# Optimization experiments

Hardware: AMD Instinct MI355X
Metric: run time of the kernel (lower is better)

Reference implementation:

```python
import jax, jax.numpy as jnp
import numpy as np

HEADS = 8
D = 1024


def setup_inputs() -> dict:
    key = jax.random.key(0)
    ks = jax.random.split(key, 10)
    B, Sq, Sk = 8, 2048, 2048
    x = jax.random.normal(ks[0], (B, Sq, D), dtype=jnp.float32)
    context = jax.random.normal(ks[1], (B, Sk, D), dtype=jnp.float32)
    # Dense params (glorot-ish scale)
    def dense(k, fin, fout):
        return jax.random.normal(k, (fin, fout), dtype=jnp.float32) / np.sqrt(fin)
    Wq = dense(ks[2], D, HEADS); bq = jnp.zeros((HEADS,), jnp.float32)
    Wk = dense(ks[3], D, HEADS); bk = jnp.zeros((HEADS,), jnp.float32)
    Wv = dense(ks[4], D, HEADS); bv = jnp.zeros((HEADS,), jnp.float32)
    Wo = dense(ks[5], HEADS, D); bo = jnp.zeros((D,), jnp.float32)
    return {"x": x, "context": context, "Wq": Wq, "bq": bq,
            "Wk": Wk, "bk": bk, "Wv": Wv, "bv": bv, "Wo": Wo, "bo": bo}


def reference(x, context, Wq, bq, Wk, bk, Wv, bv, Wo, bo):
    # q: [B,Sq,H], k/v: [B,Sk,H]  (H = heads = projection width, no head split)
    q = jnp.einsum('bsd,dh->bsh', x, Wq) + bq
    k = jnp.einsum('btd,dh->bth', context, Wk) + bk
    v = jnp.einsum('btd,dh->bth', context, Wv) + bv
    # Dot(axes=-1): scores[b,s,t] = q[b,s,:] . k[b,t,:]  -> [B,Sq,Sk]
    scores = jnp.einsum('bsh,bth->bst', q, k)
    weights = jax.nn.softmax(scores, axis=-1)  # no 1/sqrt(d) scaling in original
    # Dot(axes=(-1,1)): out[b,s,h] = sum_t weights[b,s,t] * v[b,t,h]
    out = jnp.einsum('bst,bth->bsh', weights, v)
    return jnp.einsum('bsh,hd->bsd', out, Wo) + bo
```

## Files before the change

### kernel.cpp

```cpp
#include <hip/hip_runtime.h>

constexpr int D = 1024;
constexpr int H = 8;
constexpr int S = 2048;
constexpr int B = 8;
constexpr int NROW = B * S;

__device__ __forceinline__ int swz(int i) { return i ^ ((i >> 3) & 7); }

__global__ __launch_bounds__(512)
void proj_kernel(const float* __restrict__ x, const float* __restrict__ ctx,
                 const float* __restrict__ Wq, const float* __restrict__ bq,
                 const float* __restrict__ Wk, const float* __restrict__ bk,
                 const float* __restrict__ Wv, const float* __restrict__ bv,
                 float* __restrict__ qo, float* __restrict__ ko,
                 float* __restrict__ vo)
{
    __shared__ float4 wlds[4096];
    const int tid = threadIdx.x;
    const bool kvb = (int)blockIdx.x >= (NROW / 64);
    const int blk  = kvb ? ((int)blockIdx.x - NROW / 64) : (int)blockIdx.x;

    if (!kvb) {
        const float4* w4 = (const float4*)Wq;
        for (int i = tid; i < 2048; i += 512) wlds[swz(i)] = w4[i];
    } else {
        const float4* a4 = (const float4*)Wk;
        const float4* b4 = (const float4*)Wv;
        for (int i = tid; i < 2048; i += 512) {
            wlds[swz(i)]        = a4[i];
            wlds[2048 + swz(i)] = b4[i];
        }
    }
    __syncthreads();

    const int c    = tid & 15;
    const int team = tid >> 4;
    const int row0 = blk * 64 + team * 2;
    const float* src = kvb ? ctx : x;
    const float4* r0 = (const float4*)(src + (size_t)row0 * D);
    const float4* r1 = (const float4*)(src + (size_t)(row0 + 1) * D);

    if (!kvb) {
        float a0[8], a1[8];
#pragma unroll
        for (int h = 0; h < 8; ++h) { a0[h] = 0.f; a1[h] = 0.f; }
#pragma unroll 4
        for (int j = 0; j < 16; ++j) {
            const float4 xa = r0[16 * j + c];
            const float4 xb = r1[16 * j + c];
            const int ib = 128 * j + 8 * c;
#pragma unroll
            for (int e = 0; e < 4; ++e) {
                const float4 w0 = wlds[swz(ib + 2 * e)];
                const float4 w1 = wlds[swz(ib + 2 * e + 1)];
                const float s0 = (&xa.x)[e], s1 = (&xb.x)[e];
                a0[0] += s0 * w0.x; a0[1] += s0 * w0.y; a0[2] += s0 * w0.z; a0[3] += s0 * w0.w;
                a0[4] += s0 * w1.x; a0[5] += s0 * w1.y; a0[6] += s0 * w1.z; a0[7] += s0 * w1.w;
                a1[0] += s1 * w0.x; a1[1] += s1 * w0.y; a1[2] += s1 * w0.z; a1[3] += s1 * w0.w;
                a1[4] += s1 * w1.x; a1[5] += s1 * w1.y; a1[6] += s1 * w1.z; a1[7] += s1 * w1.w;
            }
        }
#pragma unroll
        for (int h = 0; h < 8; ++h) {
            float s0 = a0[h], s1 = a1[h];
            s0 += __shfl_down(s0, 8); s1 += __shfl_down(s1, 8);
            s0 += __shfl_down(s0, 4); s1 += __shfl_down(s1, 4);
            s0 += __shfl_down(s0, 2); s1 += __shfl_down(s1, 2);
            s0 += __shfl_down(s0, 1); s1 += __shfl_down(s1, 1);
            if (c == 0) {
                qo[(size_t)row0 * H + h]       = s0 + bq[h];
                qo[(size_t)(row0 + 1) * H + h] = s1 + bq[h];
            }
        }
    } else {
        float a0[16], a1[16];
#pragma unroll
        for (int h = 0; h < 16; ++h) { a0[h] = 0.f; a1[h] = 0.f; }
#pragma unroll 2
        for (int j = 0; j < 16; ++j) {
            const float4 xa = r0[16 * j + c];
            const float4 xb = r1[16 * j + c];
            const int ib = 128 * j + 8 * c;
#pragma unroll
            for (int e = 0; e < 4; ++e) {
                const int i0 = swz(ib + 2 * e), i1 = swz(ib + 2 * e + 1);
                const float4 k0 = wlds[i0],        k1 = wlds[i1];
                const float4 v0 = wlds[2048 + i0], v1 = wlds[2048 + i1];
                const float s0 = (&xa.x)[e], s1 = (&xb.x)[e];
                a0[0]  += s0 * k0.x; a0[1]  += s0 * k0.y; a0[2]  += s0 * k0.z; a0[3]  += s0 * k0.w;
                a0[4]  += s0 * k1.x; a0[5]  += s0 * k1.y; a0[6]  += s0 * k1.z; a0[7]  += s0 * k1.w;
                a0[8]  += s0 * v0.x; a0[9]  += s0 * v0.y; a0[10] += s0 * v0.z; a0[11] += s0 * v0.w;
                a0[12] += s0 * v1.x; a0[13] += s0 * v1.y; a0[14] += s0 * v1.z; a0[15] += s0 * v1.w;
                a1[0]  += s1 * k0.x; a1[1]  += s1 * k0.y; a1[2]  += s1 * k0.z; a1[3]  += s1 * k0.w;
                a1[4]  += s1 * k1.x; a1[5]  += s1 * k1.y; a1[6]  += s1 * k1.z; a1[7]  += s1 * k1.w;
                a1[8]  += s1 * v0.x; a1[9]  += s1 * v0.y; a1[10] += s1 * v0.z; a1[11] += s1 * v0.w;
                a1[12] += s1 * v1.x; a1[13] += s1 * v1.y; a1[14] += s1 * v1.z; a1[15] += s1 * v1.w;
            }
        }
#pragma unroll
        for (int h = 0; h < 16; ++h) {
            float s0 = a0[h], s1 = a1[h];
            s0 += __shfl_down(s0, 8); s1 += __shfl_down(s1, 8);
            s0 += __shfl_down(s0, 4); s1 += __shfl_down(s1, 4);
            s0 += __shfl_down(s0, 2); s1 += __shfl_down(s1, 2);
            s0 += __shfl_down(s0, 1); s1 += __shfl_down(s1, 1);
            if (c == 0) {
                if (h < 8) {
                    ko[(size_t)row0 * H + h]       = s0 + bk[h];
                    ko[(size_t)(row0 + 1) * H + h] = s1 + bk[h];
                } else {
                    vo[(size_t)row0 * H + (h - 8)]       = s0 + bv[h - 8];
                    vo[(size_t)(row0 + 1) * H + (h - 8)] = s1 + bv[h - 8];
                }
            }
        }
    }
}

constexpr int ROWS_PER_WAVE = 4;
constexpr int ROWS_PER_BLOCK = 16;
constexpr int TILE_T = 512;

__global__ __launch_bounds__(256)
void attn_kernel(const float* __restrict__ q, const float* __restrict__ k,
                 const float* __restrict__ v, const float* __restrict__ Wo,
                 const float* __restrict__ bo, float* __restrict__ out)
{
    __shared__ float4 kt[TILE_T * 2];
    __shared__ float4 vt[TILE_T * 2];
    const int tid  = threadIdx.x;
    const int lane = tid & 63;
    const int wid  = tid >> 6;

    const int row0 = blockIdx.x * ROWS_PER_BLOCK + wid * ROWS_PER_WAVE;
    const int b = row0 >> 11;

    float qv[ROWS_PER_WAVE][H];
#pragma unroll
    for (int r = 0; r < ROWS_PER_WAVE; ++r) {
        const float4* q4 = (const float4*)(q + (size_t)(row0 + r) * H);
        const float4 a = q4[0], c = q4[1];
        qv[r][0] = a.x; qv[r][1] = a.y; qv[r][2] = a.z; qv[r][3] = a.w;
        qv[r][4] = c.x; qv[r][5] = c.y; qv[r][6] = c.z; qv[r][7] = c.w;
    }

    float l[ROWS_PER_WAVE] = {0.f, 0.f, 0.f, 0.f};
    float o[ROWS_PER_WAVE][H];
#pragma unroll
    for (int r = 0; r < ROWS_PER_WAVE; ++r)
#pragma unroll
        for (int h = 0; h < H; ++h) o[r][h] = 0.f;

    const float4* kg = (const float4*)(k + (size_t)b * S * H);
    const float4* vg = (const float4*)(v + (size_t)b * S * H);

    for (int tile = 0; tile < S / TILE_T; ++tile) {
        __syncthreads();
#pragma unroll
        for (int i = 0; i < 4; ++i) {
            kt[i * 256 + tid] = kg[tile * 1024 + i * 256 + tid];
            vt[i * 256 + tid] = vg[tile * 1024 + i * 256 + tid];
        }
        __syncthreads();
#pragma unroll 2
        for (int m = 0; m < TILE_T / 64; ++m) {
            const int t2 = (lane + (m << 6)) * 2;
            const float4 ka = kt[t2], kb = kt[t2 + 1];
            const float4 va = vt[t2], vb = vt[t2 + 1];
#pragma unroll
            for (int r = 0; r < ROWS_PER_WAVE; ++r) {
                const float s = qv[r][0] * ka.x + qv[r][1] * ka.y
                              + qv[r][2] * ka.z + qv[r][3] * ka.w
                              + qv[r][4] * kb.x + qv[r][5] * kb.y
                              + qv[r][6] * kb.z + qv[r][7] * kb.w;
                const float e = __expf(s);
                l[r] += e;
                o[r][0] += e * va.x; o[r][1] += e * va.y;
                o[r][2] += e * va.z; o[r][3] += e * va.w;
                o[r][4] += e * vb.x; o[r][5] += e * vb.y;
                o[r][6] += e * vb.z; o[r][7] += e * vb.w;
            }
        }
    }

#pragma unroll
    for (int r = 0; r < ROWS_PER_WAVE; ++r) {
#pragma unroll
        for (int off = 32; off > 0; off >>= 1) l[r] += __shfl_xor(l[r], off);
        const float inv = 1.f / l[r];
#pragma unroll
        for (int h = 0; h < H; ++h) {
#pragma unroll
            for (int off = 32; off > 0; off >>= 1) o[r][h] += __shfl_xor(o[r][h], off);
            o[r][h] *= inv;
        }
    }

    const float4* Wo4 = (const float4*)Wo;
    const float4* bo4 = (const float4*)bo;
    float4* out4 = (float4*)out;
#pragma unroll
    for (int c = 0; c < 4; ++c) {
        const int f = lane + 64 * c;
        float4 w[H];
#pragma unroll
        for (int h = 0; h < H; ++h) w[h] = Wo4[h * (D / 4) + f];
        const float4 base = bo4[f];
#pragma unroll
        for (int r = 0; r < ROWS_PER_WAVE; ++r) {
            float4 acc = base;
#pragma unroll
            for (int h = 0; h < H; ++h) {
                acc.x += o[r][h] * w[h].x;
                acc.y += o[r][h] * w[h].y;
                acc.z += o[r][h] * w[h].z;
                acc.w += o[r][h] * w[h].w;
            }
            out4[(size_t)(row0 + r) * (D / 4) + f] = acc;
        }
    }
}

extern "C" void kernel_launch(void* const* d_in, const int* in_sizes, int n_in,
                              void* d_out, int out_size, void* d_ws, size_t ws_size,
                              hipStream_t stream) {
    const float* x   = (const float*)d_in[0];
    const float* ctx = (const float*)d_in[1];
    const float* Wq  = (const float*)d_in[2];
    const float* bq  = (const float*)d_in[3];
    const float* Wk  = (const float*)d_in[4];
    const float* bk  = (const float*)d_in[5];
    const float* Wv  = (const float*)d_in[6];
    const float* bv  = (const float*)d_in[7];
    const float* Wo  = (const float*)d_in[8];
    const float* bo  = (const float*)d_in[9];
    float* out = (float*)d_out;

    float* qw = (float*)d_ws;
    float* kw = qw + (size_t)NROW * H;
    float* vw = kw + (size_t)NROW * H;

    proj_kernel<<<dim3(2 * NROW / 64), dim3(512), 0, stream>>>(
        x, ctx, Wq, bq, Wk, bk, Wv, bv, qw, kw, vw);
    attn_kernel<<<dim3(NROW / ROWS_PER_BLOCK), dim3(256), 0, stream>>>(
        qw, kw, vw, Wo, bo, out);
}
```

Measured before the change: 240.3 us.

## Split projection into uniform per-tensor blocks with four rows per team

The projection kernel now assigns each block a single tensor (Q, K or V), interleaved by block index, with 256 threads and a 32 KB weight tile instead of mixed Q and combined K/V blocks. Each 16-lane team processes four rows, accumulates into float4 registers and writes outputs with vector stores. This balances work across blocks and reduces LDS and register pressure per block. In exchange, the context tensor is now read twice, once for K and once for V, which increases global memory traffic.

Measured after the change: 238.1 us. Within noise of the previous version (-0.9%).

```diff
diff --git a/kernel.cpp b/kernel.cpp
--- a/kernel.cpp
+++ b/kernel.cpp
@@ -8,7 +8,7 @@
 
 __device__ __forceinline__ int swz(int i) { return i ^ ((i >> 3) & 7); }
 
-__global__ __launch_bounds__(512)
+__global__ __launch_bounds__(256)
 void proj_kernel(const float* __restrict__ x, const float* __restrict__ ctx,
                  const float* __restrict__ Wq, const float* __restrict__ bq,
                  const float* __restrict__ Wk, const float* __restrict__ bk,
@@ -16,104 +16,72 @@
                  float* __restrict__ qo, float* __restrict__ ko,
                  float* __restrict__ vo)
 {
-    __shared__ float4 wlds[4096];
+    __shared__ float4 wlds[2048];
     const int tid = threadIdx.x;
-    const bool kvb = (int)blockIdx.x >= (NROW / 64);
-    const int blk  = kvb ? ((int)blockIdx.x - NROW / 64) : (int)blockIdx.x;
-
-    if (!kvb) {
-        const float4* w4 = (const float4*)Wq;
-        for (int i = tid; i < 2048; i += 512) wlds[swz(i)] = w4[i];
-    } else {
-        const float4* a4 = (const float4*)Wk;
-        const float4* b4 = (const float4*)Wv;
-        for (int i = tid; i < 2048; i += 512) {
-            wlds[swz(i)]        = a4[i];
-            wlds[2048 + swz(i)] = b4[i];
-        }
+    const int tensor = (int)blockIdx.x % 3;
+    const int blk    = (int)blockIdx.x / 3;
+
+    const float* W    = (tensor == 0) ? Wq : (tensor == 1) ? Wk : Wv;
+    const float* bias = (tensor == 0) ? bq : (tensor == 1) ? bk : bv;
+    const float* src  = (tensor == 0) ? x  : ctx;
+    float*       dst  = (tensor == 0) ? qo : (tensor == 1) ? ko : vo;
+
+    {
+        const float4* w4 = (const float4*)W;
+        for (int i = tid; i < 2048; i += 256) wlds[swz(i)] = w4[i];
     }
     __syncthreads();
 
     const int c    = tid & 15;
     const int team = tid >> 4;
-    const int row0 = blk * 64 + team * 2;
-    const float* src = kvb ? ctx : x;
+    const int row0 = blk * 64 + team * 4;
     const float4* r0 = (const float4*)(src + (size_t)row0 * D);
-    const float4* r1 = (const float4*)(src + (size_t)(row0 + 1) * D);
-
-    if (!kvb) {
-        float a0[8], a1[8];
-#pragma unroll
-        for (int h = 0; h < 8; ++h) { a0[h] = 0.f; a1[h] = 0.f; }
-#pragma unroll 4
-        for (int j = 0; j < 16; ++j) {
-            const float4 xa = r0[16 * j + c];
-            const float4 xb = r1[16 * j + c];
-            const int ib = 128 * j + 8 * c;
-#pragma unroll
-            for (int e = 0; e < 4; ++e) {
-                const float4 w0 = wlds[swz(ib + 2 * e)];
-                const float4 w1 = wlds[swz(ib + 2 * e + 1)];
-                const float s0 = (&xa.x)[e], s1 = (&xb.x)[e];
-                a0[0] += s0 * w0.x; a0[1] += s0 * w0.y; a0[2] += s0 * w0.z; a0[3] += s0 * w0.w;
-                a0[4] += s0 * w1.x; a0[5] += s0 * w1.y; a0[6] += s0 * w1.z; a0[7] += s0 * w1.w;
-                a1[0] += s1 * w0.x; a1[1] += s1 * w0.y; a1[2] += s1 * w0.z; a1[3] += s1 * w0.w;
-                a1[4] += s1 * w1.x; a1[5] += s1 * w1.y; a1[6] += s1 * w1.z; a1[7] += s1 * w1.w;
+
+    float4 a0[4], a1[4];
+#pragma unroll
+    for (int r = 0; r < 4; ++r) {
+        a0[r] = make_float4(0.f, 0.f, 0.f, 0.f);
+        a1[r] = make_float4(0.f, 0.f, 0.f, 0.f);
+    }
+
+#pragma unroll 2
+    for (int j = 0; j < 16; ++j) {
+        float4 xv[4];
+#pragma unroll
+        for (int r = 0; r < 4; ++r) xv[r] = r0[r * 256 + 16 * j + c];
+        const int ib = 128 * j + 8 * c;
+#pragma unroll
+        for (int e = 0; e < 4; ++e) {
+            const float4 w0 = wlds[swz(ib + 2 * e)];
+            const float4 w1 = wlds[swz(ib + 2 * e + 1)];
+#pragma unroll
+            for (int r = 0; r < 4; ++r) {
+                const float s = (&xv[r].x)[e];
+                a0[r].x += s * w0.x; a0[r].y += s * w0.y;
+                a0[r].z += s * w0.z; a0[r].w += s * w0.w;
+                a1[r].x += s * w1.x; a1[r].y += s * w1.y;
+                a1[r].z += s * w1.z; a1[r].w += s * w1.w;
             }
         }
+    }
+
+#pragma unroll
+    for (int r = 0; r < 4; ++r) {
+        float s[8] = {a0[r].x, a0[r].y, a0[r].z, a0[r].w,
+                      a1[r].x, a1[r].y, a1[r].z, a1[r].w};
 #pragma unroll
         for (int h = 0; h < 8; ++h) {
-            float s0 = a0[h], s1 = a1[h];
-            s0 += __shfl_down(s0, 8); s1 += __shfl_down(s1, 8);
-            s0 += __shfl_down(s0, 4); s1 += __shfl_down(s1, 4);
-            s0 += __shfl_down(s0, 2); s1 += __shfl_down(s1, 2);
-            s0 += __shfl_down(s0, 1); s1 += __shfl_down(s1, 1);
-            if (c == 0) {
-                qo[(size_t)row0 * H + h]       = s0 + bq[h];
-                qo[(size_t)(row0 + 1) * H + h] = s1 + bq[h];
-            }
-        }
-    } else {
-        float a0[16], a1[16];
-#pragma unroll
-        for (int h = 0; h < 16; ++h) { a0[h] = 0.f; a1[h] = 0.f; }
-#pragma unroll 2
-        for (int j = 0; j < 16; ++j) {
-            const float4 xa = r0[16 * j + c];
-            const float4 xb = r1[16 * j + c];
-            const int ib = 128 * j + 8 * c;
-#pragma unroll
-            for (int e = 0; e < 4; ++e) {
-                const int i0 = swz(ib + 2 * e), i1 = swz(ib + 2 * e + 1);
-                const float4 k0 = wlds[i0],        k1 = wlds[i1];
-                const float4 v0 = wlds[2048 + i0], v1 = wlds[2048 + i1];
-                const float s0 = (&xa.x)[e], s1 = (&xb.x)[e];
-                a0[0]  += s0 * k0.x; a0[1]  += s0 * k0.y; a0[2]  += s0 * k0.z; a0[3]  += s0 * k0.w;
-                a0[4]  += s0 * k1.x; a0[5]  += s0 * k1.y; a0[6]  += s0 * k1.z; a0[7]  += s0 * k1.w;
-                a0[8]  += s0 * v0.x; a0[9]  += s0 * v0.y; a0[10] += s0 * v0.z; a0[11] += s0 * v0.w;
-                a0[12] += s0 * v1.x; a0[13] += s0 * v1.y; a0[14] += s0 * v1.z; a0[15] += s0 * v1.w;
-                a1[0]  += s1 * k0.x; a1[1]  += s1 * k0.y; a1[2]  += s1 * k0.z; a1[3]  += s1 * k0.w;
-                a1[4]  += s1 * k1.x; a1[5]  += s1 * k1.y; a1[6]  += s1 * k1.z; a1[7]  += s1 * k1.w;
-                a1[8]  += s1 * v0.x; a1[9]  += s1 * v0.y; a1[10] += s1 * v0.z; a1[11] += s1 * v0.w;
-                a1[12] += s1 * v1.x; a1[13] += s1 * v1.y; a1[14] += s1 * v1.z; a1[15] += s1 * v1.w;
-            }
-        }
-#pragma unroll
-        for (int h = 0; h < 16; ++h) {
-            float s0 = a0[h], s1 = a1[h];
-            s0 += __shfl_down(s0, 8); s1 += __shfl_down(s1, 8);
-            s0 += __shfl_down(s0, 4); s1 += __shfl_down(s1, 4);
-            s0 += __shfl_down(s0, 2); s1 += __shfl_down(s1, 2);
-            s0 += __shfl_down(s0, 1); s1 += __shfl_down(s1, 1);
-            if (c == 0) {
-                if (h < 8) {
-                    ko[(size_t)row0 * H + h]       = s0 + bk[h];
-                    ko[(size_t)(row0 + 1) * H + h] = s1 + bk[h];
-                } else {
-                    vo[(size_t)row0 * H + (h - 8)]       = s0 + bv[h - 8];
-                    vo[(size_t)(row0 + 1) * H + (h - 8)] = s1 + bv[h - 8];
-                }
-            }
+            s[h] += __shfl_down(s[h], 8);
+            s[h] += __shfl_down(s[h], 4);
+            s[h] += __shfl_down(s[h], 2);
+            s[h] += __shfl_down(s[h], 1);
+        }
+        if (c == 0) {
+            float4* o = (float4*)(dst + (size_t)(row0 + r) * H);
+            o[0] = make_float4(s[0] + bias[0], s[1] + bias[1],
+                               s[2] + bias[2], s[3] + bias[3]);
+            o[1] = make_float4(s[4] + bias[4], s[5] + bias[5],
+                               s[6] + bias[6], s[7] + bias[7]);
         }
     }
 }
@@ -241,7 +209,7 @@
     float* kw = qw + (size_t)NROW * H;
     float* vw = kw + (size_t)NROW * H;
 
-    proj_kernel<<<dim3(2 * NROW / 64), dim3(512), 0, stream>>>(
+    proj_kernel<<<dim3(3 * NROW / 64), dim3(256), 0, stream>>>(
         x, ctx, Wq, bq, Wk, bk, Wv, bv, qw, kw, vw);
     attn_kernel<<<dim3(NROW / ROWS_PER_BLOCK), dim3(256), 0, stream>>>(
         qw, kw, vw, Wo, bo, out);
```
